# Kernel tuning notes

Hardware: AMD Instinct MI355X
Metric: run time of the kernel (lower is better)

## Reference

```python
import jax, jax.numpy as jnp
import numpy as np

IN_FEATURES = 256
OUT_FEATURES = 256


def setup_inputs() -> dict:
    key = jax.random.key(0)
    kx, kw, ks, kb = jax.random.split(key, 4)
    x = jax.random.normal(kx, (131072, IN_FEATURES), dtype=jnp.float32)
    # Xavier-uniform init for the latent fp weight [out, in]
    limit = float(np.sqrt(6.0 / (IN_FEATURES + OUT_FEATURES)))
    W = jax.random.uniform(kw, (OUT_FEATURES, IN_FEATURES), dtype=jnp.float32,
                           minval=-limit, maxval=limit)
    # scale initialized to ones in the module; perturb slightly to make it non-trivial
    scale = jnp.ones((OUT_FEATURES,), dtype=jnp.float32) + 0.01 * jax.random.normal(ks, (OUT_FEATURES,), dtype=jnp.float32)
    bias = 0.01 * jax.random.normal(kb, (OUT_FEATURES,), dtype=jnp.float32)
    return {"x": x, "W": W, "scale": scale, "bias": bias}


def reference(x, W, scale, bias):
    # STE binarization: forward value is sign(W), gradient passes through to W
    binary_w = W + jax.lax.stop_gradient(jnp.sign(W) - W)          # [out, in]
    scaled_w = binary_w * scale[:, None]                           # per-output-channel rescale
    # F.linear(x, scaled_w, bias) = x @ scaled_w.T + bias
    return jnp.einsum('bi,oi->bo', x, scaled_w) + bias
```

## Files before the change

### kernel.cpp

```cpp
#include <hip/hip_runtime.h>
#include <hip/hip_bf16.h>


typedef __bf16 bf16_t;
typedef __attribute__((ext_vector_type(8))) __bf16 bf16x8;
typedef __attribute__((ext_vector_type(4))) float f32x4;

#define MROWS 131072
#define NDIM 256
#define KDIM 256
#define BM 64

__global__ __launch_bounds__(256) void prep_w_kernel(const float* __restrict__ W,
                                                     bf16_t* __restrict__ wb) {
    int idx = blockIdx.x * 256 + threadIdx.x;
    float w = W[idx];
    float v = (w > 0.0f) ? 1.0f : ((w < 0.0f) ? -1.0f : 0.0f);
    wb[idx] = (bf16_t)v;
}

__device__ inline bf16x8 cvt8(f32x4 lo, f32x4 hi) {
    bf16x8 r;
    r[0] = (bf16_t)lo.x; r[1] = (bf16_t)lo.y; r[2] = (bf16_t)lo.z; r[3] = (bf16_t)lo.w;
    r[4] = (bf16_t)hi.x; r[5] = (bf16_t)hi.y; r[6] = (bf16_t)hi.z; r[7] = (bf16_t)hi.w;
    return r;
}

__global__ __launch_bounds__(256) void bin_gemm_kernel(
        const float* __restrict__ x,
        const bf16_t* __restrict__ wb,
        const float* __restrict__ scale,
        const float* __restrict__ bias,
        float* __restrict__ out) {
    const int tid   = threadIdx.x;
    const int lane  = tid & 63;
    const int wave  = tid >> 6;
    const int mbase = blockIdx.x * BM;
    const int lrow  = lane & 15;
    const int lk    = lane >> 4;
    const int obase = wave * 64;

    f32x4 acc[4][4] = {};

    #pragma unroll
    for (int ks = 0; ks < 8; ++ks) {
        bf16x8 a[4], b[4];
        #pragma unroll
        for (int mi = 0; mi < 4; ++mi) {
            const float* pa = x + (size_t)(mbase + mi * 16 + lrow) * KDIM + ks * 32 + lk * 8;
            f32x4 lo = *reinterpret_cast<const f32x4*>(pa);
            f32x4 hi = *reinterpret_cast<const f32x4*>(pa + 4);
            a[mi] = cvt8(lo, hi);
        }
        #pragma unroll
        for (int ni = 0; ni < 4; ++ni) {
            const bf16_t* pb = wb + (size_t)(obase + ni * 16 + lrow) * KDIM + ks * 32 + lk * 8;
            b[ni] = *reinterpret_cast<const bf16x8*>(pb);
        }
        #pragma unroll
        for (int mi = 0; mi < 4; ++mi)
            #pragma unroll
            for (int ni = 0; ni < 4; ++ni)
                acc[mi][ni] = __builtin_amdgcn_mfma_f32_16x16x32_bf16(
                                  a[mi], b[ni], acc[mi][ni], 0, 0, 0);
    }

    float sc[4], bi[4];
    #pragma unroll
    for (int ni = 0; ni < 4; ++ni) {
        int col = obase + ni * 16 + lrow;
        sc[ni] = scale[col];
        bi[ni] = bias[col];
    }
    #pragma unroll
    for (int mi = 0; mi < 4; ++mi) {
        #pragma unroll
        for (int ni = 0; ni < 4; ++ni) {
            int col = obase + ni * 16 + lrow;
            #pragma unroll
            for (int r = 0; r < 4; ++r) {
                int row = mbase + mi * 16 + lk * 4 + r;
                __builtin_nontemporal_store(acc[mi][ni][r] * sc[ni] + bi[ni],
                                            out + (size_t)row * NDIM + col);
            }
        }
    }
}

extern "C" void kernel_launch(void* const* d_in, const int* in_sizes, int n_in,
                              void* d_out, int out_size, void* d_ws, size_t ws_size,
                              hipStream_t stream) {
    const float* x     = (const float*)d_in[0];
    const float* W     = (const float*)d_in[1];
    const float* scale = (const float*)d_in[2];
    const float* bias  = (const float*)d_in[3];
    float*       out   = (float*)d_out;
    bf16_t*      wb    = (bf16_t*)d_ws;

    prep_w_kernel<<<NDIM * KDIM / 256, 256, 0, stream>>>(W, wb);
    bin_gemm_kernel<<<MROWS / BM, 256, 0, stream>>>(x, wb, scale, bias, out);
}
```

Baseline: 299.6 us.

## Stage binarized weights in swizzled LDS and give each wave distinct rows

Each 512-thread block loads the full 256x256 bf16 sign-weight matrix into LDS with an XOR swizzle. Each of its eight waves then computes 16 rows against all 256 output columns, prefetching the next K slice of x in registers. This removes the redundant x reads across waves and the repeated global weight loads. The cost is a 128KB LDS footprint per block, which limits occupancy to about one block per CU, plus a per-block weight staging overhead. Output stores become regular stores instead of nontemporal ones.

```diff
diff --git a/kernel.cpp b/kernel.cpp
--- a/kernel.cpp
+++ b/kernel.cpp
@@ -9,7 +9,7 @@
 #define MROWS 131072
 #define NDIM 256
 #define KDIM 256
-#define BM 64
+#define BM 128
 
 __global__ __launch_bounds__(256) void prep_w_kernel(const float* __restrict__ W,
                                                      bf16_t* __restrict__ wb) {
@@ -26,63 +26,64 @@
     return r;
 }
 
-__global__ __launch_bounds__(256) void bin_gemm_kernel(
+__global__ __launch_bounds__(512, 2) void bin_gemm_kernel(
         const float* __restrict__ x,
         const bf16_t* __restrict__ wb,
         const float* __restrict__ scale,
         const float* __restrict__ bias,
         float* __restrict__ out) {
-    const int tid   = threadIdx.x;
-    const int lane  = tid & 63;
-    const int wave  = tid >> 6;
-    const int mbase = blockIdx.x * BM;
-    const int lrow  = lane & 15;
-    const int lk    = lane >> 4;
-    const int obase = wave * 64;
+    __shared__ __align__(16) char Blds[NDIM * KDIM * 2];
 
-    f32x4 acc[4][4] = {};
+    const int tid = threadIdx.x;
 
     #pragma unroll
+    for (int p = 0; p < 16; ++p) {
+        int idx16 = p * 512 + tid;
+        bf16x8 v = *reinterpret_cast<const bf16x8*>(wb + (size_t)idx16 * 8);
+        int col = idx16 >> 5;
+        int kq  = idx16 & 31;
+        int boff = col * 512 + ((kq * 16) ^ ((col & 7) << 4));
+        *reinterpret_cast<bf16x8*>(Blds + boff) = v;
+    }
+    __syncthreads();
+
+    const int lane = tid & 63;
+    const int wave = tid >> 6;
+    const int lrow = lane & 15;
+    const int lk   = lane >> 4;
+    const int r0   = blockIdx.x * BM + wave * 16;
+    const float* xrow = x + (size_t)(r0 + lrow) * KDIM + lk * 8;
+
+    f32x4 acc[16] = {};
+
+    f32x4 lo = *reinterpret_cast<const f32x4*>(xrow);
+    f32x4 hi = *reinterpret_cast<const f32x4*>(xrow + 4);
+
+    const int sw = (lrow & 7) << 4;
+    #pragma unroll
     for (int ks = 0; ks < 8; ++ks) {
-        bf16x8 a[4], b[4];
+        bf16x8 a = cvt8(lo, hi);
+        if (ks < 7) {
+            lo = *reinterpret_cast<const f32x4*>(xrow + (ks + 1) * 32);
+            hi = *reinterpret_cast<const f32x4*>(xrow + (ks + 1) * 32 + 4);
+        }
+        int t = lrow * 512 + ((ks * 64 + lk * 16) ^ sw);
         #pragma unroll
-        for (int mi = 0; mi < 4; ++mi) {
-            const float* pa = x + (size_t)(mbase + mi * 16 + lrow) * KDIM + ks * 32 + lk * 8;
-            f32x4 lo = *reinterpret_cast<const f32x4*>(pa);
-            f32x4 hi = *reinterpret_cast<const f32x4*>(pa + 4);
-            a[mi] = cvt8(lo, hi);
+        for (int ni = 0; ni < 16; ++ni) {
+            bf16x8 b = *reinterpret_cast<const bf16x8*>(Blds + ni * 8192 + t);
+            acc[ni] = __builtin_amdgcn_mfma_f32_16x16x32_bf16(a, b, acc[ni], 0, 0, 0);
         }
-        #pragma unroll
-        for (int ni = 0; ni < 4; ++ni) {
-            const bf16_t* pb = wb + (size_t)(obase + ni * 16 + lrow) * KDIM + ks * 32 + lk * 8;
-            b[ni] = *reinterpret_cast<const bf16x8*>(pb);
-        }
-        #pragma unroll
-        for (int mi = 0; mi < 4; ++mi)
-            #pragma unroll
-            for (int ni = 0; ni < 4; ++ni)
-                acc[mi][ni] = __builtin_amdgcn_mfma_f32_16x16x32_bf16(
-                                  a[mi], b[ni], acc[mi][ni], 0, 0, 0);
     }
 
-    float sc[4], bi[4];
     #pragma unroll
-    for (int ni = 0; ni < 4; ++ni) {
-        int col = obase + ni * 16 + lrow;
-        sc[ni] = scale[col];
-        bi[ni] = bias[col];
-    }
-    #pragma unroll
-    for (int mi = 0; mi < 4; ++mi) {
+    for (int ni = 0; ni < 16; ++ni) {
+        int col = ni * 16 + lrow;
+        float sc = scale[col];
+        float bi = bias[col];
         #pragma unroll
-        for (int ni = 0; ni < 4; ++ni) {
-            int col = obase + ni * 16 + lrow;
-            #pragma unroll
-            for (int r = 0; r < 4; ++r) {
-                int row = mbase + mi * 16 + lk * 4 + r;
-                __builtin_nontemporal_store(acc[mi][ni][r] * sc[ni] + bi[ni],
-                                            out + (size_t)row * NDIM + col);
-            }
+        for (int r = 0; r < 4; ++r) {
+            int row = r0 + lk * 4 + r;
+            out[(size_t)row * NDIM + col] = acc[ni][r] * sc + bi;
         }
     }
 }
@@ -98,5 +99,5 @@
     bf16_t*      wb    = (bf16_t*)d_ws;
 
     prep_w_kernel<<<NDIM * KDIM / 256, 256, 0, stream>>>(W, wb);
-    bin_gemm_kernel<<<MROWS / BM, 256, 0, stream>>>(x, wb, scale, bias, out);
+    bin_gemm_kernel<<<MROWS / BM, 512, 0, stream>>>(x, wb, scale, bias, out);
 }
```

New measurement: 246.1 us. -17.8%, faster.

## Use persistent blocks with register-resident weights and prefetched x tiles

Applied to the files above, without the earlier changes.

Switches the GEMM to a persistent grid of 256 blocks, each looping over 16-row tiles. The binarized weights for each wave's 64 columns are loaded into registers once, and the next x tile is prefetched into registers while the current one is computed. This removes the weight reloads per tile and overlaps x loads with MFMA work. The trade-offs are heavy register pressure, only 4 waves per CU across 256 CUs, and dropping nontemporal stores.

```diff
diff --git a/kernel.cpp b/kernel.cpp
--- a/kernel.cpp
+++ b/kernel.cpp
@@ -9,14 +9,15 @@
 #define MROWS 131072
 #define NDIM 256
 #define KDIM 256
-#define BM 64
+#define TROWS 16
+#define NT (MROWS / TROWS)
+#define GRID 256
 
 __global__ __launch_bounds__(256) void prep_w_kernel(const float* __restrict__ W,
                                                      bf16_t* __restrict__ wb) {
     int idx = blockIdx.x * 256 + threadIdx.x;
     float w = W[idx];
-    float v = (w > 0.0f) ? 1.0f : ((w < 0.0f) ? -1.0f : 0.0f);
-    wb[idx] = (bf16_t)v;
+    wb[idx] = (bf16_t)((w > 0.0f) ? 1.0f : ((w < 0.0f) ? -1.0f : 0.0f));
 }
 
 __device__ inline bf16x8 cvt8(f32x4 lo, f32x4 hi) {
@@ -26,63 +27,74 @@
     return r;
 }
 
-__global__ __launch_bounds__(256) void bin_gemm_kernel(
+__global__ __launch_bounds__(256, 1) void bin_gemm_kernel(
         const float* __restrict__ x,
         const bf16_t* __restrict__ wb,
         const float* __restrict__ scale,
         const float* __restrict__ bias,
         float* __restrict__ out) {
-    const int tid   = threadIdx.x;
-    const int lane  = tid & 63;
-    const int wave  = tid >> 6;
-    const int mbase = blockIdx.x * BM;
-    const int lrow  = lane & 15;
-    const int lk    = lane >> 4;
-    const int obase = wave * 64;
+    const int tid  = threadIdx.x;
+    const int lane = tid & 63;
+    const int wave = tid >> 6;
+    const int lrow = lane & 15;
+    const int lk   = lane >> 4;
+    const int cb   = wave * 64;
 
-    f32x4 acc[4][4] = {};
-
+    bf16x8 breg[4][8];
     #pragma unroll
-    for (int ks = 0; ks < 8; ++ks) {
-        bf16x8 a[4], b[4];
+    for (int ni = 0; ni < 4; ++ni) {
+        const bf16_t* pb = wb + (size_t)(cb + ni * 16 + lrow) * KDIM + lk * 8;
         #pragma unroll
-        for (int mi = 0; mi < 4; ++mi) {
-            const float* pa = x + (size_t)(mbase + mi * 16 + lrow) * KDIM + ks * 32 + lk * 8;
-            f32x4 lo = *reinterpret_cast<const f32x4*>(pa);
-            f32x4 hi = *reinterpret_cast<const f32x4*>(pa + 4);
-            a[mi] = cvt8(lo, hi);
-        }
-        #pragma unroll
-        for (int ni = 0; ni < 4; ++ni) {
-            const bf16_t* pb = wb + (size_t)(obase + ni * 16 + lrow) * KDIM + ks * 32 + lk * 8;
-            b[ni] = *reinterpret_cast<const bf16x8*>(pb);
-        }
-        #pragma unroll
-        for (int mi = 0; mi < 4; ++mi)
-            #pragma unroll
-            for (int ni = 0; ni < 4; ++ni)
-                acc[mi][ni] = __builtin_amdgcn_mfma_f32_16x16x32_bf16(
-                                  a[mi], b[ni], acc[mi][ni], 0, 0, 0);
+        for (int ks = 0; ks < 8; ++ks)
+            breg[ni][ks] = *reinterpret_cast<const bf16x8*>(pb + ks * 32);
     }
-
     float sc[4], bi[4];
     #pragma unroll
     for (int ni = 0; ni < 4; ++ni) {
-        int col = obase + ni * 16 + lrow;
-        sc[ni] = scale[col];
-        bi[ni] = bias[col];
+        sc[ni] = scale[cb + ni * 16 + lrow];
+        bi[ni] = bias[cb + ni * 16 + lrow];
     }
-    #pragma unroll
-    for (int mi = 0; mi < 4; ++mi) {
+
+    f32x4 xlo[8], xhi[8];
+    {
+        const float* p0 = x + ((size_t)blockIdx.x * TROWS + lrow) * KDIM + lk * 8;
+        #pragma unroll
+        for (int ks = 0; ks < 8; ++ks) {
+            xlo[ks] = *reinterpret_cast<const f32x4*>(p0 + ks * 32);
+            xhi[ks] = *reinterpret_cast<const f32x4*>(p0 + ks * 32 + 4);
+        }
+    }
+
+    for (int t = blockIdx.x; t < NT; t += GRID) {
+        bf16x8 a[8];
+        #pragma unroll
+        for (int ks = 0; ks < 8; ++ks) a[ks] = cvt8(xlo[ks], xhi[ks]);
+
+        int tn = t + GRID;
+        if (tn < NT) {
+            const float* pn = x + ((size_t)tn * TROWS + lrow) * KDIM + lk * 8;
+            #pragma unroll
+            for (int ks = 0; ks < 8; ++ks) {
+                xlo[ks] = *reinterpret_cast<const f32x4*>(pn + ks * 32);
+                xhi[ks] = *reinterpret_cast<const f32x4*>(pn + ks * 32 + 4);
+            }
+        }
+
+        f32x4 acc[4] = {};
+        #pragma unroll
+        for (int ks = 0; ks < 8; ++ks)
+            #pragma unroll
+            for (int ni = 0; ni < 4; ++ni)
+                acc[ni] = __builtin_amdgcn_mfma_f32_16x16x32_bf16(
+                              a[ks], breg[ni][ks], acc[ni], 0, 0, 0);
+
+        float* po = out + ((size_t)t * TROWS + lk * 4) * NDIM;
         #pragma unroll
         for (int ni = 0; ni < 4; ++ni) {
-            int col = obase + ni * 16 + lrow;
+            int col = cb + ni * 16 + lrow;
             #pragma unroll
-            for (int r = 0; r < 4; ++r) {
-                int row = mbase + mi * 16 + lk * 4 + r;
-                __builtin_nontemporal_store(acc[mi][ni][r] * sc[ni] + bi[ni],
-                                            out + (size_t)row * NDIM + col);
-            }
+            for (int r = 0; r < 4; ++r)
+                po[(size_t)r * NDIM + col] = acc[ni][r] * sc[ni] + bi[ni];
         }
     }
 }
@@ -98,5 +110,5 @@
     bf16_t*      wb    = (bf16_t*)d_ws;
 
     prep_w_kernel<<<NDIM * KDIM / 256, 256, 0, stream>>>(W, wb);
-    bin_gemm_kernel<<<MROWS / BM, 256, 0, stream>>>(x, wb, scale, bias, out);
+    bin_gemm_kernel<<<GRID, 256, 0, stream>>>(x, wb, scale, bias, out);
 }
```

Result: faster. 254.0 us (-15.2%).
